# Kernel tuning notes

Hardware: AMD Instinct MI355X
Metric: run time of the kernel (lower is better)

Reference implementation:

```python
import jax, jax.numpy as jnp
import numpy as np
from jax.ops import segment_sum, segment_max

N_M = 100000   # muon nodes
N_J = 100000   # jet nodes
E   = 1600000  # edges per relation (~avg degree 16)
D   = 64       # input feature dim
H   = 64       # hidden_channels
C   = 2        # num_classes

def setup_inputs():
    key = jax.random.key(0)
    ks = jax.random.split(key, 16)
    g = lambda k, shape, fan: jax.random.normal(k, shape, jnp.float32) / np.sqrt(fan).astype(np.float32)
    return {
        "x_muons": jax.random.normal(ks[0], (N_M, D), jnp.float32),
        "x_jets":  jax.random.normal(ks[1], (N_J, D), jnp.float32),
        "ei_mm": jax.random.randint(ks[2], (2, E), 0, N_M, jnp.int32),
        "ei_mj": jnp.stack([jax.random.randint(ks[3], (E,), 0, N_M, jnp.int32),
                            jax.random.randint(ks[4], (E,), 0, N_J, jnp.int32)]),
        "ei_jj": jax.random.randint(ks[5], (2, E), 0, N_J, jnp.int32),
        "gat_w_src": g(ks[6], (D, H), D),
        "gat_w_dst": g(ks[7], (D, H), D),
        "gat_att_src": g(ks[8], (H,), H),
        "gat_att_dst": g(ks[9], (H,), H),
        "gat_bias": jnp.zeros((H,), jnp.float32),
        "sage_w_l": g(ks[10], (D, H), D),
        "sage_w_r": g(ks[11], (D, H), D),
        "sage_bias": jnp.zeros((H,), jnp.float32),
        "gcn_w": g(ks[12], (D, H), D),
        "gcn_bias": jnp.zeros((H,), jnp.float32),
        "lin_w": g(ks[13], (H, C), H),
        "lin_b": jnp.zeros((C,), jnp.float32),
    }

def _add_self_loops(ei, n):
    loop = jnp.arange(n, dtype=ei.dtype)
    return jnp.concatenate([ei[0], loop]), jnp.concatenate([ei[1], loop])

def _gat(x, ei, w_src, w_dst, att_src, att_dst, bias):
    # PyG GATConv, heads=1, add_self_loops=True, negative_slope=0.2
    n = x.shape[0]
    src, dst = _add_self_loops(ei, n)
    hs = x @ w_src                      # [n, H] source-side messages
    hd = x @ w_dst                      # dst-side (attention only)
    a = jax.nn.leaky_relu((hs @ att_src)[src] + (hd @ att_dst)[dst], 0.2)
    m = segment_max(a, dst, num_segments=n)      # per-dst softmax (stable)
    ea = jnp.exp(a - m[dst])
    z = segment_sum(ea, dst, num_segments=n)
    alpha = ea / z[dst]                 # self loop guarantees z > 0
    return segment_sum(alpha[:, None] * hs[src], dst, num_segments=n) + bias

def _sage(x_src, x_dst, ei, w_l, w_r, bias):
    # PyG SAGEConv: mean aggregation, root weight, no self loops
    n = x_dst.shape[0]
    src, dst = ei[0], ei[1]
    agg = segment_sum(x_src[src], dst, num_segments=n)
    cnt = segment_sum(jnp.ones_like(dst, jnp.float32), dst, num_segments=n)
    mean = agg / jnp.maximum(cnt, 1.0)[:, None]
    return mean @ w_l + x_dst @ w_r + bias

def _gcn(x, ei, w, bias):
    # PyG GCNConv: symmetric gcn_norm on A + I
    n = x.shape[0]
    src, dst = _add_self_loops(ei, n)
    xw = x @ w
    deg = segment_sum(jnp.ones_like(dst, jnp.float32), dst, num_segments=n)
    dis = deg ** -0.5                   # deg >= 1 due to self loops
    norm = dis[src] * dis[dst]
    return segment_sum(norm[:, None] * xw[src], dst, num_segments=n) + bias

def reference(x_muons, x_jets, ei_mm, ei_mj, ei_jj,
              gat_w_src, gat_w_dst, gat_att_src, gat_att_dst, gat_bias,
              sage_w_l, sage_w_r, sage_bias, gcn_w, gcn_bias, lin_w, lin_b):
    # Original forward returns inside the layer loop -> exactly one HeteroConv layer runs.
    muons = _gat(x_muons, ei_mm, gat_w_src, gat_w_dst, gat_att_src, gat_att_dst, gat_bias)
    jets = (_sage(x_muons, x_jets, ei_mj, sage_w_l, sage_w_r, sage_bias)
            + _gcn(x_jets, ei_jj, gcn_w, gcn_bias))   # HeteroConv aggr='sum' on dst type 'jets'
    muons = jax.nn.relu(muons)
    jets = jax.nn.relu(jets)
    out = jnp.concatenate([muons, jets], axis=0)       # [N_M + N_J, H]
    return jax.nn.sigmoid(out @ lin_w + lin_b)
```

## Files before the change

kernel.cpp:

```cpp
#include <hip/hip_runtime.h>
#include <math.h>

#define N_M 100000
#define N_J 100000
#define NE  1600000
#define NTOT (3*N_M)
#define ETOT (3*NE)
#define NB_SCAN 293
#define DD  64
#define HH  64

#define NBIN 586
#define BIN_SHIFT 9
#define G1 640
#define EPB ((ETOT + G1 - 1) / G1)

__device__ __forceinline__ float lrelu(float a){ return fmaxf(a, 0.2f*a); }
__device__ __forceinline__ float wmax(float v){
    #pragma unroll
    for (int o = 32; o; o >>= 1) v = fmaxf(v, __shfl_xor(v, o));
    return v;
}
__device__ __forceinline__ float wsum(float v){
    #pragma unroll
    for (int o = 32; o; o >>= 1) v += __shfl_xor(v, o);
    return v;
}
__device__ __forceinline__ float sigm(float x){ return 1.f/(1.f + expf(-x)); }

__device__ __forceinline__ unsigned ford(float f){
    unsigned b = __float_as_uint(f);
    return (b & 0x80000000u) ? ~b : (b | 0x80000000u);
}
__device__ __forceinline__ float funord(unsigned u){
    return (u & 0x80000000u) ? __uint_as_float(u & 0x7fffffffu) : __uint_as_float(~u);
}

__device__ __forceinline__ unsigned short f2bf(float f){
    unsigned u = __float_as_uint(f);
    u += 0x7FFFu + ((u >> 16) & 1u);
    return (unsigned short)(u >> 16);
}
__device__ __forceinline__ float bf2f(unsigned short h){
    return __uint_as_float((unsigned)h << 16);
}


__global__ __launch_bounds__(256) void k_muon_prep(
    const float* __restrict__ x, const float* __restrict__ w_src,
    const float* __restrict__ w_dst, const float* __restrict__ att_src,
    const float* __restrict__ att_dst,
    unsigned short* __restrict__ hs_b, float* __restrict__ as_, float* __restrict__ ad_,
    unsigned short* __restrict__ xm_b, unsigned* __restrict__ maxAs_u)
{
    __shared__ float lw[DD*HH];
    __shared__ float latt[HH];
    __shared__ float lvd[DD];
    __shared__ float lred[4];
    int tid = threadIdx.x;
    for (int i = tid; i < DD*HH; i += 256) lw[i] = w_src[i];
    if (tid < HH) latt[tid] = att_src[tid];
    if (tid < DD){
        float s = 0.f;
        #pragma unroll 8
        for (int h = 0; h < HH; ++h) s += w_dst[tid*HH + h] * att_dst[h];
        lvd[tid] = s;
    }
    __syncthreads();
    int row = blockIdx.x*64 + (tid >> 2);
    int q = tid & 3;
    bool live = (row < N_M);
    float asp = -1e30f, adp = 0.f;
    if (live){
        const float4* x4 = (const float4*)(x + (size_t)row*DD);
        float acc[16];
        #pragma unroll
        for (int f = 0; f < 16; ++f) acc[f] = 0.f;
        for (int kk = 0; kk < 16; ++kk){
            float4 xv = x4[kk];
            adp += xv.x*lvd[4*kk] + xv.y*lvd[4*kk+1] + xv.z*lvd[4*kk+2] + xv.w*lvd[4*kk+3];
            if ((kk >> 2) == q)
                *(ushort4*)(xm_b + (size_t)row*DD + 4*kk) =
                    make_ushort4(f2bf(xv.x), f2bf(xv.y), f2bf(xv.z), f2bf(xv.w));
            float xs[4] = {xv.x, xv.y, xv.z, xv.w};
            #pragma unroll
            for (int j = 0; j < 4; ++j){
                const float* wp = lw + (4*kk + j)*HH + (q << 4);
                float xk = xs[j];
                #pragma unroll
                for (int f = 0; f < 16; ++f) acc[f] = fmaf(xk, wp[f], acc[f]);
            }
        }
        float a = 0.f;
        #pragma unroll
        for (int f = 0; f < 16; ++f) a += acc[f] * latt[(q<<4) + f];
        a += __shfl_xor(a, 1);
        a += __shfl_xor(a, 2);
        asp = a;
        unsigned short* hp = hs_b + (size_t)row*HH + (q << 4);
        #pragma unroll
        for (int j = 0; j < 4; ++j)
            ((ushort4*)hp)[j] = make_ushort4(f2bf(acc[4*j]), f2bf(acc[4*j+1]),
                                             f2bf(acc[4*j+2]), f2bf(acc[4*j+3]));
        if (q == 0){ as_[row] = asp; ad_[row] = adp; }
    }
    float bm = wmax(asp);
    if ((tid & 63) == 0) lred[tid >> 6] = bm;
    __syncthreads();
    if (tid == 0){
        float m = fmaxf(fmaxf(lred[0], lred[1]), fmaxf(lred[2], lred[3]));
        atomicMax(maxAs_u, ford(m));
    }
}

__global__ __launch_bounds__(512) void k_jet_prep(
    const float* __restrict__ x, const float* __restrict__ gcn_w,
    const float* __restrict__ w_r, const float* __restrict__ sb,
    const float* __restrict__ gb,
    unsigned short* __restrict__ xw_b, float* __restrict__ xr)
{
    __shared__ float lwg[DD*HH];
    __shared__ float lwr[DD*HH];
    __shared__ float lb[HH];
    int tid = threadIdx.x;
    for (int i = tid; i < DD*HH; i += 512){ lwg[i] = gcn_w[i]; lwr[i] = w_r[i]; }
    if (tid < HH) lb[tid] = sb[tid] + gb[tid];
    __syncthreads();
    int row = blockIdx.x*128 + (tid >> 2);
    int q = tid & 3;
    if (row >= N_J) return;
    const float4* x4 = (const float4*)(x + (size_t)row*DD);
    float accg[16], accr[16];
    #pragma unroll
    for (int f = 0; f < 16; ++f){ accg[f] = 0.f; accr[f] = 0.f; }
    for (int kk = 0; kk < 16; ++kk){
        float4 xv = x4[kk];
        float xs[4] = {xv.x, xv.y, xv.z, xv.w};
        #pragma unroll
        for (int j = 0; j < 4; ++j){
            const float* wg = lwg + (4*kk + j)*HH + (q << 4);
            const float* wr = lwr + (4*kk + j)*HH + (q << 4);
            float xk = xs[j];
            #pragma unroll
            for (int f = 0; f < 16; ++f){
                accg[f] = fmaf(xk, wg[f], accg[f]);
                accr[f] = fmaf(xk, wr[f], accr[f]);
            }
        }
    }
    unsigned short* hp = xw_b + (size_t)row*HH + (q << 4);
    float* rp = xr + (size_t)row*HH + (q << 4);
    #pragma unroll
    for (int j = 0; j < 4; ++j){
        ((ushort4*)hp)[j] = make_ushort4(f2bf(accg[4*j]), f2bf(accg[4*j+1]),
                                         f2bf(accg[4*j+2]), f2bf(accg[4*j+3]));
        int f0 = (q << 4) + 4*j;
        ((float4*)rp)[j] = make_float4(accr[4*j]   + lb[f0],
                                       accr[4*j+1] + lb[f0+1],
                                       accr[4*j+2] + lb[f0+2],
                                       accr[4*j+3] + lb[f0+3]);
    }
}


__device__ __forceinline__ void edge_rd(int t, const int* ei_mm, const int* ei_mj,
                                        const int* ei_jj, const int** ei, int* r, int* e){
    if (t < NE){ *r = 0; *e = t; *ei = ei_mm; }
    else if (t < 2*NE){ *r = 1; *e = t - NE; *ei = ei_mj; }
    else { *r = 2; *e = t - 2*NE; *ei = ei_jj; }
}

__global__ __launch_bounds__(256) void k_bin0(
    const int* __restrict__ ei_mm, const int* __restrict__ ei_mj,
    const int* __restrict__ ei_jj, int* __restrict__ g_bincnt)
{
    __shared__ int bh[NBIN];
    int tid = threadIdx.x;
    for (int i = tid; i < NBIN; i += 256) bh[i] = 0;
    __syncthreads();
    int t0 = blockIdx.x * EPB;
    int t1 = min(t0 + EPB, ETOT);
    for (int t = t0 + tid; t < t1; t += 256){
        const int* ei; int r, e;
        edge_rd(t, ei_mm, ei_mj, ei_jj, &ei, &r, &e);
        int bucket = r*N_M + ei[NE + e];
        atomicAdd(&bh[bucket >> BIN_SHIFT], 1);
    }
    __syncthreads();
    for (int i = tid; i < NBIN; i += 256)
        if (bh[i]) atomicAdd(&g_bincnt[i], bh[i]);
}

__global__ void k_binscan(const int* __restrict__ g_bincnt, int* __restrict__ g_binoff,
                          int* __restrict__ g_bincur, int* __restrict__ offs)
{
    int l = threadIdx.x;
    int base = l * 10;
    int v[10]; int s = 0;
    #pragma unroll
    for (int k = 0; k < 10; ++k){
        int idx = base + k;
        v[k] = (idx < NBIN) ? g_bincnt[idx] : 0;
        s += v[k];
    }
    int inc = s;
    #pragma unroll
    for (int o = 1; o < 64; o <<= 1){
        int u = __shfl_up(inc, o);
        if (l >= o) inc += u;
    }
    int ex = inc - s;
    #pragma unroll
    for (int k = 0; k < 10; ++k){
        int idx = base + k;
        if (idx < NBIN){ g_binoff[idx] = ex; g_bincur[idx] = ex; ex += v[k]; }
    }
    if (l == 63) g_binoff[NBIN] = ex;
    if (l == 0)  offs[NTOT] = ETOT;
}

__global__ __launch_bounds__(256) void k_bin1(
    const int* __restrict__ ei_mm, const int* __restrict__ ei_mj,
    const int* __restrict__ ei_jj, int* __restrict__ g_bincur,
    unsigned* __restrict__ binned)
{
    __shared__ int bh[NBIN];
    __shared__ int cb[NBIN];
    int tid = threadIdx.x;
    for (int i = tid; i < NBIN; i += 256) bh[i] = 0;
    __syncthreads();
    int t0 = blockIdx.x * EPB;
    int t1 = min(t0 + EPB, ETOT);
    for (int t = t0 + tid; t < t1; t += 256){
        const int* ei; int r, e;
        edge_rd(t, ei_mm, ei_mj, ei_jj, &ei, &r, &e);
        int bucket = r*N_M + ei[NE + e];
        atomicAdd(&bh[bucket >> BIN_SHIFT], 1);
    }
    __syncthreads();
    for (int i = tid; i < NBIN; i += 256){
        int c = bh[i];
        cb[i] = c ? atomicAdd(&g_bincur[i], c) : 0;
        bh[i] = 0;
    }
    __syncthreads();
    for (int t = t0 + tid; t < t1; t += 256){
        const int* ei; int r, e;
        edge_rd(t, ei_mm, ei_mj, ei_jj, &ei, &r, &e);
        int s = ei[e];
        int bucket = r*N_M + ei[NE + e];
        int bin = bucket >> BIN_SHIFT;
        int lb  = bucket & 511;
        int pos = cb[bin] + atomicAdd(&bh[bin], 1);
        binned[pos] = ((unsigned)lb << 17) | (unsigned)s;
    }
}

__global__ __launch_bounds__(256) void k_build(
    const unsigned* __restrict__ binned, const int* __restrict__ g_binoff,
    int* __restrict__ offs, int* __restrict__ perm, float* __restrict__ dis)
{
    __shared__ int lh[512];
    __shared__ int lcur[512];
    __shared__ int ls[256];
    int b = blockIdx.x, tid = threadIdx.x;
    int e0 = g_binoff[b], e1 = g_binoff[b+1];
    lh[tid] = 0; lh[tid + 256] = 0;
    __syncthreads();
    for (int e = e0 + tid; e < e1; e += 256)
        atomicAdd(&lh[binned[e] >> 17], 1);
    __syncthreads();
    int a0 = lh[2*tid], a1 = lh[2*tid + 1];
    int s = a0 + a1;
    ls[tid] = s; __syncthreads();
    for (int o = 1; o < 256; o <<= 1){
        int u = (tid >= o) ? ls[tid - o] : 0;
        __syncthreads();
        ls[tid] += u;
        __syncthreads();
    }
    int ex = ls[tid] - s;
    lcur[2*tid]     = ex;
    lcur[2*tid + 1] = ex + a0;
    int gb = b*512 + 2*tid;
    if (gb     < NTOT) offs[gb]     = e0 + ex;
    if (gb + 1 < NTOT) offs[gb + 1] = e0 + ex + a0;
    if (gb     >= 2*N_M && gb     < NTOT) dis[gb     - 2*N_M] = rsqrtf((float)a0 + 1.f);
    if (gb + 1 >= 2*N_M && gb + 1 < NTOT) dis[gb + 1 - 2*N_M] = rsqrtf((float)a1 + 1.f);
    __syncthreads();
    for (int e = e0 + tid; e < e1; e += 256){
        unsigned p = binned[e];
        int pos = atomicAdd(&lcur[p >> 17], 1);
        perm[e0 + pos] = (int)(p & 0x1FFFFu);
    }
}


__global__ void k_hist(const int* __restrict__ ei_mm, const int* __restrict__ ei_mj,
                       const int* __restrict__ ei_jj, int* __restrict__ cnt){
    int t = blockIdx.x*256 + threadIdx.x;
    if (t >= ETOT) return;
    const int* ei; int r, e;
    edge_rd(t, ei_mm, ei_mj, ei_jj, &ei, &r, &e);
    atomicAdd(&cnt[r*N_M + ei[NE + e]], 1);
}

__global__ __launch_bounds__(256) void k_scan1(const int* __restrict__ cnt,
                                               int* __restrict__ offs, int* __restrict__ bsum){
    __shared__ int ls[256];
    int b = blockIdx.x, t = threadIdx.x;
    int base = b*1024 + t*4;
    int4 c = make_int4(0,0,0,0);
    if (base < NTOT) c = *(const int4*)(cnt + base);
    int s = c.x + c.y + c.z + c.w;
    ls[t] = s; __syncthreads();
    for (int o = 1; o < 256; o <<= 1){
        int a = (t >= o) ? ls[t - o] : 0;
        __syncthreads();
        ls[t] += a;
        __syncthreads();
    }
    int excl = ls[t] - s;
    if (t == 255) bsum[b] = ls[255];
    if (base < NTOT){
        offs[base]   = excl;
        offs[base+1] = excl + c.x;
        offs[base+2] = excl + c.x + c.y;
        offs[base+3] = excl + c.x + c.y + c.z;
    }
}

__global__ __launch_bounds__(512) void k_scan2(int* __restrict__ bsum){
    __shared__ int ls[512];
    int t = threadIdx.x;
    int v = (t < NB_SCAN) ? bsum[t] : 0;
    ls[t] = v; __syncthreads();
    for (int o = 1; o < 512; o <<= 1){
        int a = (t >= o) ? ls[t - o] : 0;
        __syncthreads();
        ls[t] += a;
        __syncthreads();
    }
    if (t < NB_SCAN) bsum[t] = ls[t] - v;
}

__global__ void k_scan3(int* __restrict__ offs, const int* __restrict__ bsum){
    int b = blockIdx.x, t = threadIdx.x;
    int base = b*1024 + t*4;
    if (base >= NTOT) return;
    int add = bsum[b];
    int4* p = (int4*)(offs + base);
    int4 v = *p;
    v.x += add; v.y += add; v.z += add; v.w += add;
    *p = v;
}

__global__ void k_fill(const int* __restrict__ ei_mm, const int* __restrict__ ei_mj,
                       const int* __restrict__ ei_jj, const int* __restrict__ offs,
                       int* __restrict__ cursor, int* __restrict__ perm){
    int t = blockIdx.x*256 + threadIdx.x;
    if (t >= ETOT) return;
    const int* ei; int r, e;
    edge_rd(t, ei_mm, ei_mj, ei_jj, &ei, &r, &e);
    int s = ei[e];
    int bkt = r*N_M + ei[NE + e];
    int pos = atomicAdd(&cursor[bkt], 1);
    perm[offs[bkt] + pos] = s;
}

__global__ void k_set_offs_top(int* __restrict__ offs){ offs[NTOT] = ETOT; }

__global__ void k_dis(const int* __restrict__ offs, float* __restrict__ dis){
    int j = blockIdx.x*256 + threadIdx.x;
    if (j >= N_J) return;
    int beg = offs[2*N_M + j];
    int end = (j == N_J-1) ? ETOT : offs[2*N_M + j + 1];
    dis[j] = rsqrtf((float)(end - beg + 1));
}


__global__ __launch_bounds__(512) void k_out(
    const unsigned short* __restrict__ xm_b, const unsigned short* __restrict__ xw_b,
    const float* __restrict__ xr, const float* __restrict__ dis,
    const int* __restrict__ offs, const int* __restrict__ perm,
    const float* __restrict__ as_, const float* __restrict__ ad_,
    const unsigned short* __restrict__ hs_b, const unsigned* __restrict__ maxAs_u,
    const float* __restrict__ gat_bias, const float* __restrict__ w_l,
    const float* __restrict__ lin_w, const float* __restrict__ lin_b,
    float* __restrict__ out)
{
    int tid = threadIdx.x;
    int wid = tid >> 6;
    int l = tid & 63;
    int p = l & 15, g = l >> 4;
    int b = blockIdx.x;
    if (b & 1){
        int d = (b >> 1)*8 + wid;
        if (d >= N_M) return;
        int beg = offs[d], end = offs[d+1];
        float ad_d = ad_[d];
        float M = lrelu(funord(*maxAs_u) + ad_d);
        float a_self = lrelu(as_[d] + ad_d);
        float zl = 0.f;
        float acc0 = 0.f, acc1 = 0.f, acc2 = 0.f, acc3 = 0.f;
        for (int base = beg; base < end; base += 64){
            int e = base + l;
            int sB = 0; float eaB = 0.f;
            if (e < end){
                sB = perm[e];
                eaB = expf(lrelu(as_[sB] + ad_d) - M);
            }
            zl += eaB;
            int cc = min(64, end - base);
            int k = 0;
            for (; k + 32 <= cc; k += 32){
                #pragma unroll
                for (int qq = 0; qq < 8; ++qq){
                    int idx = k + qq*4 + g;
                    int s = __shfl(sB, idx);
                    float w = __shfl(eaB, idx);
                    ushort4 v = *(const ushort4*)(hs_b + (size_t)s*HH + 4*p);
                    acc0 = fmaf(w, bf2f(v.x), acc0);
                    acc1 = fmaf(w, bf2f(v.y), acc1);
                    acc2 = fmaf(w, bf2f(v.z), acc2);
                    acc3 = fmaf(w, bf2f(v.w), acc3);
                }
            }
            for (; k < cc; k += 4){
                int idx = k + g;
                int cl = min(idx, cc - 1);
                int s = __shfl(sB, cl);
                float w = __shfl(eaB, cl);
                if (idx >= cc) w = 0.f;
                ushort4 v = *(const ushort4*)(hs_b + (size_t)s*HH + 4*p);
                acc0 = fmaf(w, bf2f(v.x), acc0);
                acc1 = fmaf(w, bf2f(v.y), acc1);
                acc2 = fmaf(w, bf2f(v.z), acc2);
                acc3 = fmaf(w, bf2f(v.w), acc3);
            }
        }
        float z = wsum(zl);
        acc0 += __shfl_xor(acc0, 16); acc0 += __shfl_xor(acc0, 32);
        acc1 += __shfl_xor(acc1, 16); acc1 += __shfl_xor(acc1, 32);
        acc2 += __shfl_xor(acc2, 16); acc2 += __shfl_xor(acc2, 32);
        acc3 += __shfl_xor(acc3, 16); acc3 += __shfl_xor(acc3, 32);
        float eself = expf(a_self - M);
        z += eself;
        ushort4 hv = *(const ushort4*)(hs_b + (size_t)d*HH + 4*p);
        acc0 = fmaf(eself, bf2f(hv.x), acc0);
        acc1 = fmaf(eself, bf2f(hv.y), acc1);
        acc2 = fmaf(eself, bf2f(hv.z), acc2);
        acc3 = fmaf(eself, bf2f(hv.w), acc3);
        float rz = 1.f / z;
        float q0 = 0.f, q1 = 0.f;
        {
            float a[4] = {acc0, acc1, acc2, acc3};
            #pragma unroll
            for (int c = 0; c < 4; ++c){
                int f = 4*p + c;
                float v2 = fmaxf(a[c]*rz + gat_bias[f], 0.f);
                q0 = fmaf(v2, lin_w[f*2 + 0], q0);
                q1 = fmaf(v2, lin_w[f*2 + 1], q1);
            }
        }
        #pragma unroll
        for (int o = 1; o <= 8; o <<= 1){ q0 += __shfl_xor(q0, o); q1 += __shfl_xor(q1, o); }
        if (l == 0){
            size_t oo = (size_t)d*2;
            out[oo]   = sigm(q0 + lin_b[0]);
            out[oo+1] = sigm(q1 + lin_b[1]);
        }
    } else {
        int j = (b >> 1)*8 + wid;
        if (j >= N_J) return;
        int beg1 = offs[N_M + j],  end1 = offs[N_M + j + 1];
        int beg2 = offs[2*N_M + j];
        int end2 = (j == N_J-1) ? ETOT : offs[2*N_M + j + 1];
        float dj = dis[j];
        float sa0 = 0.f, sa1 = 0.f, sa2 = 0.f, sa3 = 0.f;
        float gc0 = 0.f, gc1 = 0.f, gc2 = 0.f, gc3 = 0.f;
        for (int b1 = beg1, b2 = beg2; b1 < end1 || b2 < end2; b1 += 64, b2 += 64){
            int e1 = b1 + l, e2 = b2 + l;
            bool h1 = (b1 < end1), h2 = (b2 < end2);
            int sB1 = 0, sB2 = 0; float nB2 = 0.f;
            if (h1 && e1 < end1) sB1 = perm[e1];
            if (h2 && e2 < end2){ sB2 = perm[e2]; nB2 = dis[sB2]*dj; }
            if (h1){
                int cc = min(64, end1 - b1);
                int k = 0;
                for (; k + 16 <= cc; k += 16){
                    #pragma unroll
                    for (int qq = 0; qq < 4; ++qq){
                        int idx = k + qq*4 + g;
                        int s = __shfl(sB1, idx);
                        ushort4 v = *(const ushort4*)(xm_b + (size_t)s*DD + 4*p);
                        sa0 += bf2f(v.x); sa1 += bf2f(v.y); sa2 += bf2f(v.z); sa3 += bf2f(v.w);
                    }
                }
                for (; k < cc; k += 4){
                    int idx = k + g;
                    int cl = min(idx, cc - 1);
                    int s = __shfl(sB1, cl);
                    float w = (idx < cc) ? 1.f : 0.f;
                    ushort4 v = *(const ushort4*)(xm_b + (size_t)s*DD + 4*p);
                    sa0 = fmaf(w, bf2f(v.x), sa0);
                    sa1 = fmaf(w, bf2f(v.y), sa1);
                    sa2 = fmaf(w, bf2f(v.z), sa2);
                    sa3 = fmaf(w, bf2f(v.w), sa3);
                }
            }
            if (h2){
                int cc = min(64, end2 - b2);
                int k = 0;
                for (; k + 16 <= cc; k += 16){
                    #pragma unroll
                    for (int qq = 0; qq < 4; ++qq){
                        int idx = k + qq*4 + g;
                        int s = __shfl(sB2, idx);
                        float w = __shfl(nB2, idx);
                        ushort4 v = *(const ushort4*)(xw_b + (size_t)s*HH + 4*p);
                        gc0 = fmaf(w, bf2f(v.x), gc0);
                        gc1 = fmaf(w, bf2f(v.y), gc1);
                        gc2 = fmaf(w, bf2f(v.z), gc2);
                        gc3 = fmaf(w, bf2f(v.w), gc3);
                    }
                }
                for (; k < cc; k += 4){
                    int idx = k + g;
                    int cl = min(idx, cc - 1);
                    int s = __shfl(sB2, cl);
                    float w = __shfl(nB2, cl);
                    if (idx >= cc) w = 0.f;
                    ushort4 v = *(const ushort4*)(xw_b + (size_t)s*HH + 4*p);
                    gc0 = fmaf(w, bf2f(v.x), gc0);
                    gc1 = fmaf(w, bf2f(v.y), gc1);
                    gc2 = fmaf(w, bf2f(v.z), gc2);
                    gc3 = fmaf(w, bf2f(v.w), gc3);
                }
            }
        }
        sa0 += __shfl_xor(sa0, 16); sa0 += __shfl_xor(sa0, 32);
        sa1 += __shfl_xor(sa1, 16); sa1 += __shfl_xor(sa1, 32);
        sa2 += __shfl_xor(sa2, 16); sa2 += __shfl_xor(sa2, 32);
        sa3 += __shfl_xor(sa3, 16); sa3 += __shfl_xor(sa3, 32);
        gc0 += __shfl_xor(gc0, 16); gc0 += __shfl_xor(gc0, 32);
        gc1 += __shfl_xor(gc1, 16); gc1 += __shfl_xor(gc1, 32);
        gc2 += __shfl_xor(gc2, 16); gc2 += __shfl_xor(gc2, 32);
        gc3 += __shfl_xor(gc3, 16); gc3 += __shfl_xor(gc3, 32);
        float inv = (end1 > beg1) ? 1.f/(float)(end1 - beg1) : 1.f;
        float mean_a[4] = {sa0*inv, sa1*inv, sa2*inv, sa3*inv};
        {
            ushort4 sv = *(const ushort4*)(xw_b + (size_t)j*HH + 4*p);
            float djj = dj*dj;
            gc0 = fmaf(djj, bf2f(sv.x), gc0);
            gc1 = fmaf(djj, bf2f(sv.y), gc1);
            gc2 = fmaf(djj, bf2f(sv.z), gc2);
            gc3 = fmaf(djj, bf2f(sv.w), gc3);
        }
        float b0 = __shfl(gc0, l >> 2), b1 = __shfl(gc1, l >> 2);
        float b2 = __shfl(gc2, l >> 2), b3 = __shfl(gc3, l >> 2);
        int c2 = l & 3;
        float accg_lin = (c2 == 0) ? b0 : ((c2 == 1) ? b1 : ((c2 == 2) ? b2 : b3));
        float xacc = 0.f;
        #pragma unroll
        for (int k = 0; k < 64; ++k){
            float mk = __shfl(mean_a[k & 3], k >> 2);
            xacc = fmaf(mk, w_l[k*64 + l], xacc);
        }
        float v2 = fmaxf(xacc + accg_lin + xr[(size_t)j*HH + l], 0.f);
        float q0 = wsum(v2 * lin_w[l*2 + 0]);
        float q1 = wsum(v2 * lin_w[l*2 + 1]);
        if (l == 0){
            size_t oo = (size_t)(N_M + j)*2;
            out[oo]   = sigm(q0 + lin_b[0]);
            out[oo+1] = sigm(q1 + lin_b[1]);
        }
    }
}

extern "C" void kernel_launch(void* const* d_in, const int* in_sizes, int n_in,
                              void* d_out, int out_size, void* d_ws, size_t ws_size,
                              hipStream_t stream) {
    const float* x_muons   = (const float*)d_in[0];
    const float* x_jets    = (const float*)d_in[1];
    const int*   ei_mm     = (const int*)d_in[2];
    const int*   ei_mj     = (const int*)d_in[3];
    const int*   ei_jj     = (const int*)d_in[4];
    const float* gat_w_src = (const float*)d_in[5];
    const float* gat_w_dst = (const float*)d_in[6];
    const float* gat_att_s = (const float*)d_in[7];
    const float* gat_att_d = (const float*)d_in[8];
    const float* gat_bias  = (const float*)d_in[9];
    const float* sage_w_l  = (const float*)d_in[10];
    const float* sage_w_r  = (const float*)d_in[11];
    const float* sage_bias = (const float*)d_in[12];
    const float* gcn_w     = (const float*)d_in[13];
    const float* gcn_bias  = (const float*)d_in[14];
    const float* lin_w     = (const float*)d_in[15];
    const float* lin_b     = (const float*)d_in[16];
    float* out = (float*)d_out;

    float* ws = (float*)d_ws;
    size_t o = 0;
    unsigned short* hs_b = (unsigned short*)(ws + o); o += (size_t)N_M*HH/2;
    unsigned short* xw_b = (unsigned short*)(ws + o); o += (size_t)N_J*HH/2;
    unsigned short* xm_b = (unsigned short*)(ws + o); o += (size_t)N_M*DD/2;
    float* xr    = ws + o; o += (size_t)N_J*HH;
    float* as_   = ws + o; o += N_M;
    float* ad_   = ws + o; o += N_M;
    float* dis   = ws + o; o += N_J;
    unsigned* maxAs_u = (unsigned*)(ws + o); o += 16;
    int* offs   = (int*)(ws + o); o += NTOT + 4;
    int* perm   = (int*)(ws + o); o += ETOT;
    size_t o_common = o;

    int nb64_m = (N_M + 63) / 64;

    hipMemsetAsync(maxAs_u, 0, sizeof(unsigned), stream);
    k_muon_prep<<<nb64_m, 256, 0, stream>>>(x_muons, gat_w_src, gat_w_dst,
                                            gat_att_s, gat_att_d,
                                            hs_b, as_, ad_, xm_b, maxAs_u);
    k_jet_prep<<<(N_J + 127)/128, 512, 0, stream>>>(x_jets, gcn_w, sage_w_r, sage_bias,
                                                    gcn_bias, xw_b, xr);

    size_t need_fast = (o_common + ETOT + 3*NBIN + 16) * sizeof(float);
    if (ws_size >= need_fast){
        unsigned* binned = (unsigned*)(ws + o); o += ETOT;
        int* g_bincnt    = (int*)(ws + o); o += NBIN;
        int* g_binoff    = (int*)(ws + o); o += NBIN + 4;
        int* g_bincur    = (int*)(ws + o); o += NBIN;
        hipMemsetAsync(g_bincnt, 0, NBIN*sizeof(int), stream);
        k_bin0<<<G1, 256, 0, stream>>>(ei_mm, ei_mj, ei_jj, g_bincnt);
        k_binscan<<<1, 64, 0, stream>>>(g_bincnt, g_binoff, g_bincur, offs);
        k_bin1<<<G1, 256, 0, stream>>>(ei_mm, ei_mj, ei_jj, g_bincur, binned);
        k_build<<<NBIN, 256, 0, stream>>>(binned, g_binoff, offs, perm, dis);
    } else {
        int* cnt    = (int*)(ws + o); o += NTOT;
        int* cursor = (int*)(ws + o); o += NTOT;
        int* bsum   = (int*)(ws + o); o += 512;
        hipMemsetAsync(cnt,    0, (size_t)NTOT*sizeof(int), stream);
        hipMemsetAsync(cursor, 0, (size_t)NTOT*sizeof(int), stream);
        int nbE3 = (ETOT + 255) / 256;
        k_hist<<<nbE3, 256, 0, stream>>>(ei_mm, ei_mj, ei_jj, cnt);
        k_scan1<<<NB_SCAN, 256, 0, stream>>>(cnt, offs, bsum);
        k_scan2<<<1, 512, 0, stream>>>(bsum);
        k_scan3<<<NB_SCAN, 256, 0, stream>>>(offs, bsum);
        k_fill<<<nbE3, 256, 0, stream>>>(ei_mm, ei_mj, ei_jj, offs, cursor, perm);
        k_set_offs_top<<<1, 1, 0, stream>>>(offs);
        k_dis<<<(N_J + 255)/256, 256, 0, stream>>>(offs, dis);
    }

    int nb_out = 2 * ((N_M + 7)/8);
    k_out<<<nb_out, 512, 0, stream>>>(xm_b, xw_b, xr, dis, offs, perm,
                                      as_, ad_, hs_b, maxAs_u,
                                      gat_bias, sage_w_l, lin_w, lin_b, out);
}
```

Baseline: 487.1 us.

## Replace atomic bin counting with per-block count matrix and split output kernel

```diff
diff --git a/kernel.cpp b/kernel.cpp
--- a/kernel.cpp
+++ b/kernel.cpp
@@ -170,15 +170,16 @@
     else { *r = 2; *e = t - 2*NE; *ei = ei_jj; }
 }
 
-__global__ __launch_bounds__(256) void k_bin0(
+__global__ __launch_bounds__(256) void k_binmat(
     const int* __restrict__ ei_mm, const int* __restrict__ ei_mj,
-    const int* __restrict__ ei_jj, int* __restrict__ g_bincnt)
+    const int* __restrict__ ei_jj, int* __restrict__ mat)
 {
     __shared__ int bh[NBIN];
     int tid = threadIdx.x;
     for (int i = tid; i < NBIN; i += 256) bh[i] = 0;
     __syncthreads();
-    int t0 = blockIdx.x * EPB;
+    int b = blockIdx.x;
+    int t0 = b * EPB;
     int t1 = min(t0 + EPB, ETOT);
     for (int t = t0 + tid; t < t1; t += 256){
         const int* ei; int r, e;
@@ -187,12 +188,36 @@
         atomicAdd(&bh[bucket >> BIN_SHIFT], 1);
     }
     __syncthreads();
-    for (int i = tid; i < NBIN; i += 256)
-        if (bh[i]) atomicAdd(&g_bincnt[i], bh[i]);
-}
-
-__global__ void k_binscan(const int* __restrict__ g_bincnt, int* __restrict__ g_binoff,
-                          int* __restrict__ g_bincur, int* __restrict__ offs)
+    for (int i = tid; i < NBIN; i += 256) mat[b*NBIN + i] = bh[i];
+}
+
+__global__ void k_colscan(int* __restrict__ mat, int* __restrict__ bintot)
+{
+    int bin = blockIdx.x;
+    int l = threadIdx.x;
+    int v[10]; int s = 0;
+    #pragma unroll
+    for (int k = 0; k < 10; ++k){
+        v[k] = mat[(l*10 + k)*NBIN + bin];
+        s += v[k];
+    }
+    int inc = s;
+    #pragma unroll
+    for (int o = 1; o < 64; o <<= 1){
+        int u = __shfl_up(inc, o);
+        if (l >= o) inc += u;
+    }
+    int ex = inc - s;
+    #pragma unroll
+    for (int k = 0; k < 10; ++k){
+        mat[(l*10 + k)*NBIN + bin] = ex;
+        ex += v[k];
+    }
+    if (l == 63) bintot[bin] = inc;
+}
+
+__global__ void k_binscan(const int* __restrict__ bintot, int* __restrict__ g_binoff,
+                          int* __restrict__ offs)
 {
     int l = threadIdx.x;
     int base = l * 10;
@@ -200,7 +225,7 @@
     #pragma unroll
     for (int k = 0; k < 10; ++k){
         int idx = base + k;
-        v[k] = (idx < NBIN) ? g_bincnt[idx] : 0;
+        v[k] = (idx < NBIN) ? bintot[idx] : 0;
         s += v[k];
     }
     int inc = s;
@@ -213,7 +238,7 @@
     #pragma unroll
     for (int k = 0; k < 10; ++k){
         int idx = base + k;
-        if (idx < NBIN){ g_binoff[idx] = ex; g_bincur[idx] = ex; ex += v[k]; }
+        if (idx < NBIN){ g_binoff[idx] = ex; ex += v[k]; }
     }
     if (l == 63) g_binoff[NBIN] = ex;
     if (l == 0)  offs[NTOT] = ETOT;
@@ -221,29 +246,20 @@
 
 __global__ __launch_bounds__(256) void k_bin1(
     const int* __restrict__ ei_mm, const int* __restrict__ ei_mj,
-    const int* __restrict__ ei_jj, int* __restrict__ g_bincur,
-    unsigned* __restrict__ binned)
+    const int* __restrict__ ei_jj, const int* __restrict__ g_binoff,
+    const int* __restrict__ mat, unsigned* __restrict__ binned)
 {
     __shared__ int bh[NBIN];
     __shared__ int cb[NBIN];
     int tid = threadIdx.x;
-    for (int i = tid; i < NBIN; i += 256) bh[i] = 0;
-    __syncthreads();
-    int t0 = blockIdx.x * EPB;
+    int b = blockIdx.x;
+    for (int i = tid; i < NBIN; i += 256){
+        cb[i] = g_binoff[i] + mat[b*NBIN + i];
+        bh[i] = 0;
+    }
+    __syncthreads();
+    int t0 = b * EPB;
     int t1 = min(t0 + EPB, ETOT);
-    for (int t = t0 + tid; t < t1; t += 256){
-        const int* ei; int r, e;
-        edge_rd(t, ei_mm, ei_mj, ei_jj, &ei, &r, &e);
-        int bucket = r*N_M + ei[NE + e];
-        atomicAdd(&bh[bucket >> BIN_SHIFT], 1);
-    }
-    __syncthreads();
-    for (int i = tid; i < NBIN; i += 256){
-        int c = bh[i];
-        cb[i] = c ? atomicAdd(&g_bincur[i], c) : 0;
-        bh[i] = 0;
-    }
-    __syncthreads();
     for (int t = t0 + tid; t < t1; t += 256){
         const int* ei; int r, e;
         edge_rd(t, ei_mm, ei_mj, ei_jj, &ei, &r, &e);
@@ -379,59 +395,41 @@
 }
 
 
-__global__ __launch_bounds__(512) void k_out(
-    const unsigned short* __restrict__ xm_b, const unsigned short* __restrict__ xw_b,
-    const float* __restrict__ xr, const float* __restrict__ dis,
+__global__ __launch_bounds__(512) void k_muon_gat_out(
     const int* __restrict__ offs, const int* __restrict__ perm,
     const float* __restrict__ as_, const float* __restrict__ ad_,
     const unsigned short* __restrict__ hs_b, const unsigned* __restrict__ maxAs_u,
-    const float* __restrict__ gat_bias, const float* __restrict__ w_l,
+    const float* __restrict__ gat_bias,
     const float* __restrict__ lin_w, const float* __restrict__ lin_b,
     float* __restrict__ out)
 {
-    int tid = threadIdx.x;
-    int wid = tid >> 6;
-    int l = tid & 63;
+    int wid = threadIdx.x >> 6;
+    int l = threadIdx.x & 63;
+    int d = blockIdx.x*8 + wid;
+    if (d >= N_M) return;
     int p = l & 15, g = l >> 4;
-    int b = blockIdx.x;
-    if (b & 1){
-        int d = (b >> 1)*8 + wid;
-        if (d >= N_M) return;
-        int beg = offs[d], end = offs[d+1];
-        float ad_d = ad_[d];
-        float M = lrelu(funord(*maxAs_u) + ad_d);
-        float a_self = lrelu(as_[d] + ad_d);
-        float zl = 0.f;
-        float acc0 = 0.f, acc1 = 0.f, acc2 = 0.f, acc3 = 0.f;
-        for (int base = beg; base < end; base += 64){
-            int e = base + l;
-            int sB = 0; float eaB = 0.f;
-            if (e < end){
-                sB = perm[e];
-                eaB = expf(lrelu(as_[sB] + ad_d) - M);
-            }
-            zl += eaB;
-            int cc = min(64, end - base);
-            int k = 0;
-            for (; k + 32 <= cc; k += 32){
-                #pragma unroll
-                for (int qq = 0; qq < 8; ++qq){
-                    int idx = k + qq*4 + g;
-                    int s = __shfl(sB, idx);
-                    float w = __shfl(eaB, idx);
-                    ushort4 v = *(const ushort4*)(hs_b + (size_t)s*HH + 4*p);
-                    acc0 = fmaf(w, bf2f(v.x), acc0);
-                    acc1 = fmaf(w, bf2f(v.y), acc1);
-                    acc2 = fmaf(w, bf2f(v.z), acc2);
-                    acc3 = fmaf(w, bf2f(v.w), acc3);
-                }
-            }
-            for (; k < cc; k += 4){
-                int idx = k + g;
-                int cl = min(idx, cc - 1);
-                int s = __shfl(sB, cl);
-                float w = __shfl(eaB, cl);
-                if (idx >= cc) w = 0.f;
+    int beg = offs[d], end = offs[d+1];
+    float ad_d = ad_[d];
+    float M = lrelu(funord(*maxAs_u) + ad_d);
+    float a_self = lrelu(as_[d] + ad_d);
+    float zl = 0.f;
+    float acc0 = 0.f, acc1 = 0.f, acc2 = 0.f, acc3 = 0.f;
+    for (int base = beg; base < end; base += 64){
+        int e = base + l;
+        int sB = 0; float eaB = 0.f;
+        if (e < end){
+            sB = perm[e];
+            eaB = expf(lrelu(as_[sB] + ad_d) - M);
+        }
+        zl += eaB;
+        int cc = min(64, end - base);
+        int k = 0;
+        for (; k + 32 <= cc; k += 32){
+            #pragma unroll
+            for (int qq = 0; qq < 8; ++qq){
+                int idx = k + qq*4 + g;
+                int s = __shfl(sB, idx);
+                float w = __shfl(eaB, idx);
                 ushort4 v = *(const ushort4*)(hs_b + (size_t)s*HH + 4*p);
                 acc0 = fmaf(w, bf2f(v.x), acc0);
                 acc1 = fmaf(w, bf2f(v.y), acc1);
@@ -439,98 +437,114 @@
                 acc3 = fmaf(w, bf2f(v.w), acc3);
             }
         }
-        float z = wsum(zl);
-        acc0 += __shfl_xor(acc0, 16); acc0 += __shfl_xor(acc0, 32);
-        acc1 += __shfl_xor(acc1, 16); acc1 += __shfl_xor(acc1, 32);
-        acc2 += __shfl_xor(acc2, 16); acc2 += __shfl_xor(acc2, 32);
-        acc3 += __shfl_xor(acc3, 16); acc3 += __shfl_xor(acc3, 32);
-        float eself = expf(a_self - M);
-        z += eself;
-        ushort4 hv = *(const ushort4*)(hs_b + (size_t)d*HH + 4*p);
-        acc0 = fmaf(eself, bf2f(hv.x), acc0);
-        acc1 = fmaf(eself, bf2f(hv.y), acc1);
-        acc2 = fmaf(eself, bf2f(hv.z), acc2);
-        acc3 = fmaf(eself, bf2f(hv.w), acc3);
-        float rz = 1.f / z;
-        float q0 = 0.f, q1 = 0.f;
-        {
-            float a[4] = {acc0, acc1, acc2, acc3};
-            #pragma unroll
-            for (int c = 0; c < 4; ++c){
-                int f = 4*p + c;
-                float v2 = fmaxf(a[c]*rz + gat_bias[f], 0.f);
-                q0 = fmaf(v2, lin_w[f*2 + 0], q0);
-                q1 = fmaf(v2, lin_w[f*2 + 1], q1);
-            }
-        }
+        for (; k < cc; k += 4){
+            int idx = k + g;
+            int cl = min(idx, cc - 1);
+            int s = __shfl(sB, cl);
+            float w = __shfl(eaB, cl);
+            if (idx >= cc) w = 0.f;
+            ushort4 v = *(const ushort4*)(hs_b + (size_t)s*HH + 4*p);
+            acc0 = fmaf(w, bf2f(v.x), acc0);
+            acc1 = fmaf(w, bf2f(v.y), acc1);
+            acc2 = fmaf(w, bf2f(v.z), acc2);
+            acc3 = fmaf(w, bf2f(v.w), acc3);
+        }
+    }
+    float z = wsum(zl);
+    acc0 += __shfl_xor(acc0, 16); acc0 += __shfl_xor(acc0, 32);
+    acc1 += __shfl_xor(acc1, 16); acc1 += __shfl_xor(acc1, 32);
+    acc2 += __shfl_xor(acc2, 16); acc2 += __shfl_xor(acc2, 32);
+    acc3 += __shfl_xor(acc3, 16); acc3 += __shfl_xor(acc3, 32);
+    float eself = expf(a_self - M);
+    z += eself;
+    ushort4 hv = *(const ushort4*)(hs_b + (size_t)d*HH + 4*p);
+    acc0 = fmaf(eself, bf2f(hv.x), acc0);
+    acc1 = fmaf(eself, bf2f(hv.y), acc1);
+    acc2 = fmaf(eself, bf2f(hv.z), acc2);
+    acc3 = fmaf(eself, bf2f(hv.w), acc3);
+    float rz = 1.f / z;
+    float q0 = 0.f, q1 = 0.f;
+    {
+        float a[4] = {acc0, acc1, acc2, acc3};
         #pragma unroll
-        for (int o = 1; o <= 8; o <<= 1){ q0 += __shfl_xor(q0, o); q1 += __shfl_xor(q1, o); }
-        if (l == 0){
-            size_t oo = (size_t)d*2;
-            out[oo]   = sigm(q0 + lin_b[0]);
-            out[oo+1] = sigm(q1 + lin_b[1]);
-        }
-    } else {
-        int j = (b >> 1)*8 + wid;
-        if (j >= N_J) return;
-        int beg1 = offs[N_M + j],  end1 = offs[N_M + j + 1];
-        int beg2 = offs[2*N_M + j];
-        int end2 = (j == N_J-1) ? ETOT : offs[2*N_M + j + 1];
-        float dj = dis[j];
-        float sa0 = 0.f, sa1 = 0.f, sa2 = 0.f, sa3 = 0.f;
-        float gc0 = 0.f, gc1 = 0.f, gc2 = 0.f, gc3 = 0.f;
-        for (int b1 = beg1, b2 = beg2; b1 < end1 || b2 < end2; b1 += 64, b2 += 64){
-            int e1 = b1 + l, e2 = b2 + l;
-            bool h1 = (b1 < end1), h2 = (b2 < end2);
-            int sB1 = 0, sB2 = 0; float nB2 = 0.f;
-            if (h1 && e1 < end1) sB1 = perm[e1];
-            if (h2 && e2 < end2){ sB2 = perm[e2]; nB2 = dis[sB2]*dj; }
-            if (h1){
-                int cc = min(64, end1 - b1);
-                int k = 0;
-                for (; k + 16 <= cc; k += 16){
-                    #pragma unroll
-                    for (int qq = 0; qq < 4; ++qq){
-                        int idx = k + qq*4 + g;
-                        int s = __shfl(sB1, idx);
-                        ushort4 v = *(const ushort4*)(xm_b + (size_t)s*DD + 4*p);
-                        sa0 += bf2f(v.x); sa1 += bf2f(v.y); sa2 += bf2f(v.z); sa3 += bf2f(v.w);
-                    }
-                }
-                for (; k < cc; k += 4){
-                    int idx = k + g;
-                    int cl = min(idx, cc - 1);
-                    int s = __shfl(sB1, cl);
-                    float w = (idx < cc) ? 1.f : 0.f;
+        for (int c = 0; c < 4; ++c){
+            int f = 4*p + c;
+            float v2 = fmaxf(a[c]*rz + gat_bias[f], 0.f);
+            q0 = fmaf(v2, lin_w[f*2 + 0], q0);
+            q1 = fmaf(v2, lin_w[f*2 + 1], q1);
+        }
+    }
+    #pragma unroll
+    for (int o = 1; o <= 8; o <<= 1){ q0 += __shfl_xor(q0, o); q1 += __shfl_xor(q1, o); }
+    if (l == 0){
+        size_t oo = (size_t)d*2;
+        out[oo]   = sigm(q0 + lin_b[0]);
+        out[oo+1] = sigm(q1 + lin_b[1]);
+    }
+}
+
+__global__ __launch_bounds__(512) void k_jet_out(
+    const unsigned short* __restrict__ xm_b, const unsigned short* __restrict__ xw_b,
+    const float* __restrict__ xr, const float* __restrict__ dis,
+    const int* __restrict__ offs, const int* __restrict__ perm,
+    const float* __restrict__ w_l,
+    const float* __restrict__ lin_w, const float* __restrict__ lin_b,
+    float* __restrict__ out)
+{
+    __shared__ float lwl[DD*HH];
+    int tid = threadIdx.x;
+    for (int i = tid; i < DD*HH; i += 512) lwl[i] = w_l[i];
+    __syncthreads();
+    int wid = tid >> 6;
+    int l = tid & 63;
+    int j = blockIdx.x*8 + wid;
+    if (j >= N_J) return;
+    int p = l & 15, g = l >> 4;
+    int beg1 = offs[N_M + j],  end1 = offs[N_M + j + 1];
+    int beg2 = offs[2*N_M + j];
+    int end2 = (j == N_J-1) ? ETOT : offs[2*N_M + j + 1];
+    float dj = dis[j];
+    float sa0 = 0.f, sa1 = 0.f, sa2 = 0.f, sa3 = 0.f;
+    float gc0 = 0.f, gc1 = 0.f, gc2 = 0.f, gc3 = 0.f;
+    for (int b1 = beg1, b2 = beg2; b1 < end1 || b2 < end2; b1 += 64, b2 += 64){
+        int e1 = b1 + l, e2 = b2 + l;
+        bool h1 = (b1 < end1), h2 = (b2 < end2);
+        int sB1 = 0, sB2 = 0; float nB2 = 0.f;
+        if (h1 && e1 < end1) sB1 = perm[e1];
+        if (h2 && e2 < end2){ sB2 = perm[e2]; nB2 = dis[sB2]*dj; }
+        if (h1){
+            int cc = min(64, end1 - b1);
+            int k = 0;
+            for (; k + 16 <= cc; k += 16){
+                #pragma unroll
+                for (int qq = 0; qq < 4; ++qq){
+                    int idx = k + qq*4 + g;
+                    int s = __shfl(sB1, idx);
                     ushort4 v = *(const ushort4*)(xm_b + (size_t)s*DD + 4*p);
-                    sa0 = fmaf(w, bf2f(v.x), sa0);
-                    sa1 = fmaf(w, bf2f(v.y), sa1);
-                    sa2 = fmaf(w, bf2f(v.z), sa2);
-                    sa3 = fmaf(w, bf2f(v.w), sa3);
+                    sa0 += bf2f(v.x); sa1 += bf2f(v.y); sa2 += bf2f(v.z); sa3 += bf2f(v.w);
                 }
             }
-            if (h2){
-                int cc = min(64, end2 - b2);
-                int k = 0;
-                for (; k + 16 <= cc; k += 16){
-                    #pragma unroll
-                    for (int qq = 0; qq < 4; ++qq){
-                        int idx = k + qq*4 + g;
-                        int s = __shfl(sB2, idx);
-                        float w = __shfl(nB2, idx);
-                        ushort4 v = *(const ushort4*)(xw_b + (size_t)s*HH + 4*p);
-                        gc0 = fmaf(w, bf2f(v.x), gc0);
-                        gc1 = fmaf(w, bf2f(v.y), gc1);
-                        gc2 = fmaf(w, bf2f(v.z), gc2);
-                        gc3 = fmaf(w, bf2f(v.w), gc3);
-                    }
-                }
-                for (; k < cc; k += 4){
-                    int idx = k + g;
-                    int cl = min(idx, cc - 1);
-                    int s = __shfl(sB2, cl);
-                    float w = __shfl(nB2, cl);
-                    if (idx >= cc) w = 0.f;
+            for (; k < cc; k += 4){
+                int idx = k + g;
+                int cl = min(idx, cc - 1);
+                int s = __shfl(sB1, cl);
+                float w = (idx < cc) ? 1.f : 0.f;
+                ushort4 v = *(const ushort4*)(xm_b + (size_t)s*DD + 4*p);
+                sa0 = fmaf(w, bf2f(v.x), sa0);
+                sa1 = fmaf(w, bf2f(v.y), sa1);
+                sa2 = fmaf(w, bf2f(v.z), sa2);
+                sa3 = fmaf(w, bf2f(v.w), sa3);
+            }
+        }
+        if (h2){
+            int cc = min(64, end2 - b2);
+            int k = 0;
+            for (; k + 16 <= cc; k += 16){
+                #pragma unroll
+                for (int qq = 0; qq < 4; ++qq){
+                    int idx = k + qq*4 + g;
+                    int s = __shfl(sB2, idx);
+                    float w = __shfl(nB2, idx);
                     ushort4 v = *(const ushort4*)(xw_b + (size_t)s*HH + 4*p);
                     gc0 = fmaf(w, bf2f(v.x), gc0);
                     gc1 = fmaf(w, bf2f(v.y), gc1);
@@ -538,43 +552,55 @@
                     gc3 = fmaf(w, bf2f(v.w), gc3);
                 }
             }
-        }
-        sa0 += __shfl_xor(sa0, 16); sa0 += __shfl_xor(sa0, 32);
-        sa1 += __shfl_xor(sa1, 16); sa1 += __shfl_xor(sa1, 32);
-        sa2 += __shfl_xor(sa2, 16); sa2 += __shfl_xor(sa2, 32);
-        sa3 += __shfl_xor(sa3, 16); sa3 += __shfl_xor(sa3, 32);
-        gc0 += __shfl_xor(gc0, 16); gc0 += __shfl_xor(gc0, 32);
-        gc1 += __shfl_xor(gc1, 16); gc1 += __shfl_xor(gc1, 32);
-        gc2 += __shfl_xor(gc2, 16); gc2 += __shfl_xor(gc2, 32);
-        gc3 += __shfl_xor(gc3, 16); gc3 += __shfl_xor(gc3, 32);
-        float inv = (end1 > beg1) ? 1.f/(float)(end1 - beg1) : 1.f;
-        float mean_a[4] = {sa0*inv, sa1*inv, sa2*inv, sa3*inv};
-        {
-            ushort4 sv = *(const ushort4*)(xw_b + (size_t)j*HH + 4*p);
-            float djj = dj*dj;
-            gc0 = fmaf(djj, bf2f(sv.x), gc0);
-            gc1 = fmaf(djj, bf2f(sv.y), gc1);
-            gc2 = fmaf(djj, bf2f(sv.z), gc2);
-            gc3 = fmaf(djj, bf2f(sv.w), gc3);
-        }
-        float b0 = __shfl(gc0, l >> 2), b1 = __shfl(gc1, l >> 2);
-        float b2 = __shfl(gc2, l >> 2), b3 = __shfl(gc3, l >> 2);
-        int c2 = l & 3;
-        float accg_lin = (c2 == 0) ? b0 : ((c2 == 1) ? b1 : ((c2 == 2) ? b2 : b3));
-        float xacc = 0.f;
-        #pragma unroll
-        for (int k = 0; k < 64; ++k){
-            float mk = __shfl(mean_a[k & 3], k >> 2);
-            xacc = fmaf(mk, w_l[k*64 + l], xacc);
-        }
-        float v2 = fmaxf(xacc + accg_lin + xr[(size_t)j*HH + l], 0.f);
-        float q0 = wsum(v2 * lin_w[l*2 + 0]);
-        float q1 = wsum(v2 * lin_w[l*2 + 1]);
-        if (l == 0){
-            size_t oo = (size_t)(N_M + j)*2;
-            out[oo]   = sigm(q0 + lin_b[0]);
-            out[oo+1] = sigm(q1 + lin_b[1]);
-        }
+            for (; k < cc; k += 4){
+                int idx = k + g;
+                int cl = min(idx, cc - 1);
+                int s = __shfl(sB2, cl);
+                float w = __shfl(nB2, cl);
+                if (idx >= cc) w = 0.f;
+                ushort4 v = *(const ushort4*)(xw_b + (size_t)s*HH + 4*p);
+                gc0 = fmaf(w, bf2f(v.x), gc0);
+                gc1 = fmaf(w, bf2f(v.y), gc1);
+                gc2 = fmaf(w, bf2f(v.z), gc2);
+                gc3 = fmaf(w, bf2f(v.w), gc3);
+            }
+        }
+    }
+    sa0 += __shfl_xor(sa0, 16); sa0 += __shfl_xor(sa0, 32);
+    sa1 += __shfl_xor(sa1, 16); sa1 += __shfl_xor(sa1, 32);
+    sa2 += __shfl_xor(sa2, 16); sa2 += __shfl_xor(sa2, 32);
+    sa3 += __shfl_xor(sa3, 16); sa3 += __shfl_xor(sa3, 32);
+    gc0 += __shfl_xor(gc0, 16); gc0 += __shfl_xor(gc0, 32);
+    gc1 += __shfl_xor(gc1, 16); gc1 += __shfl_xor(gc1, 32);
+    gc2 += __shfl_xor(gc2, 16); gc2 += __shfl_xor(gc2, 32);
+    gc3 += __shfl_xor(gc3, 16); gc3 += __shfl_xor(gc3, 32);
+    float inv = (end1 > beg1) ? 1.f/(float)(end1 - beg1) : 1.f;
+    float mean_a[4] = {sa0*inv, sa1*inv, sa2*inv, sa3*inv};
+    {
+        ushort4 sv = *(const ushort4*)(xw_b + (size_t)j*HH + 4*p);
+        float djj = dj*dj;
+        gc0 = fmaf(djj, bf2f(sv.x), gc0);
+        gc1 = fmaf(djj, bf2f(sv.y), gc1);
+        gc2 = fmaf(djj, bf2f(sv.z), gc2);
+        gc3 = fmaf(djj, bf2f(sv.w), gc3);
+    }
+    float b0 = __shfl(gc0, l >> 2), b1 = __shfl(gc1, l >> 2);
+    float b2 = __shfl(gc2, l >> 2), b3 = __shfl(gc3, l >> 2);
+    int c2 = l & 3;
+    float accg_lin = (c2 == 0) ? b0 : ((c2 == 1) ? b1 : ((c2 == 2) ? b2 : b3));
+    float xacc = 0.f;
+    #pragma unroll
+    for (int k = 0; k < 64; ++k){
+        float mk = __shfl(mean_a[k & 3], k >> 2);
+        xacc = fmaf(mk, lwl[k*64 + l], xacc);
+    }
+    float v2 = fmaxf(xacc + accg_lin + xr[(size_t)j*HH + l], 0.f);
+    float q0 = wsum(v2 * lin_w[l*2 + 0]);
+    float q1 = wsum(v2 * lin_w[l*2 + 1]);
+    if (l == 0){
+        size_t oo = (size_t)(N_M + j)*2;
+        out[oo]   = sigm(q0 + lin_b[0]);
+        out[oo+1] = sigm(q1 + lin_b[1]);
     }
 }
 
@@ -623,16 +649,16 @@
     k_jet_prep<<<(N_J + 127)/128, 512, 0, stream>>>(x_jets, gcn_w, sage_w_r, sage_bias,
                                                     gcn_bias, xw_b, xr);
 
-    size_t need_fast = (o_common + ETOT + 3*NBIN + 16) * sizeof(float);
+    size_t need_fast = (o_common + ETOT + (size_t)G1*NBIN + 2*NBIN + 32) * sizeof(float);
     if (ws_size >= need_fast){
         unsigned* binned = (unsigned*)(ws + o); o += ETOT;
-        int* g_bincnt    = (int*)(ws + o); o += NBIN;
+        int* mat         = (int*)(ws + o); o += (size_t)G1*NBIN;
+        int* bintot      = (int*)(ws + o); o += NBIN + 4;
         int* g_binoff    = (int*)(ws + o); o += NBIN + 4;
-        int* g_bincur    = (int*)(ws + o); o += NBIN;
-        hipMemsetAsync(g_bincnt, 0, NBIN*sizeof(int), stream);
-        k_bin0<<<G1, 256, 0, stream>>>(ei_mm, ei_mj, ei_jj, g_bincnt);
-        k_binscan<<<1, 64, 0, stream>>>(g_bincnt, g_binoff, g_bincur, offs);
-        k_bin1<<<G1, 256, 0, stream>>>(ei_mm, ei_mj, ei_jj, g_bincur, binned);
+        k_binmat<<<G1, 256, 0, stream>>>(ei_mm, ei_mj, ei_jj, mat);
+        k_colscan<<<NBIN, 64, 0, stream>>>(mat, bintot);
+        k_binscan<<<1, 64, 0, stream>>>(bintot, g_binoff, offs);
+        k_bin1<<<G1, 256, 0, stream>>>(ei_mm, ei_mj, ei_jj, g_binoff, mat, binned);
         k_build<<<NBIN, 256, 0, stream>>>(binned, g_binoff, offs, perm, dis);
     } else {
         int* cnt    = (int*)(ws + o); o += NTOT;
@@ -650,8 +676,8 @@
         k_dis<<<(N_J + 255)/256, 256, 0, stream>>>(offs, dis);
     }
 
-    int nb_out = 2 * ((N_M + 7)/8);
-    k_out<<<nb_out, 512, 0, stream>>>(xm_b, xw_b, xr, dis, offs, perm,
-                                      as_, ad_, hs_b, maxAs_u,
-                                      gat_bias, sage_w_l, lin_w, lin_b, out);
-}
+    k_muon_gat_out<<<(N_M + 7)/8, 512, 0, stream>>>(offs, perm, as_, ad_, hs_b, maxAs_u,
+                                                    gat_bias, lin_w, lin_b, out);
+    k_jet_out<<<(N_J + 7)/8, 512, 0, stream>>>(xm_b, xw_b, xr, dis, offs, perm,
+                                               sage_w_l, lin_w, lin_b, out);
+}
```

After: 430.3 us. 11.7% less time.
